# Kernel tuning notes

Measured on AMD Instinct MI355X. Metric: run time of the kernel, lower is better.

Reference implementation:

```python
import jax, jax.numpy as jnp
import numpy as np

NUM_USERS = 50000
NUM_ITEMS = 50000
LATENT_DIM = 64
NUM_INTERACTIONS = 1600000
N_LAYERS = 4  # 4 ODE blocks, euler 1-step each == 4 LightGCN propagations


def setup_inputs() -> dict:
    key = jax.random.key(0)
    k1, k2, k3, k4, k5 = jax.random.split(key, 5)
    user_emb = 0.1 * jax.random.normal(k1, (NUM_USERS, LATENT_DIM), dtype=jnp.float32)
    item_emb = 0.1 * jax.random.normal(k2, (NUM_ITEMS, LATENT_DIM), dtype=jnp.float32)
    eu = jax.random.randint(k3, (NUM_INTERACTIONS,), 0, NUM_USERS, dtype=jnp.int32)
    ei = jax.random.randint(jax.random.fold_in(k3, 1), (NUM_INTERACTIONS,), 0, NUM_ITEMS, dtype=jnp.int32)
    edge_index = jnp.stack([eu, ei])  # [2, E] user->item interactions
    users = jax.random.randint(k4, (4096,), 0, NUM_USERS, dtype=jnp.int32)
    items = jax.random.randint(k5, (4096,), 0, NUM_ITEMS, dtype=jnp.int32)
    return {"user_emb": user_emb, "item_emb": item_emb,
            "edge_index": edge_index, "users": users, "items": items}


def _graph(edge_index):
    # Symmetric bipartite graph over n_users + n_items nodes, normalized D^-1/2 A D^-1/2.
    eu, ei = edge_index[0], edge_index[1] + NUM_USERS
    rows = jnp.concatenate([eu, ei])
    cols = jnp.concatenate([ei, eu])
    n = NUM_USERS + NUM_ITEMS
    deg = jax.ops.segment_sum(jnp.ones_like(rows, dtype=jnp.float32), rows, num_segments=n)
    dinv = jnp.where(deg > 0, jax.lax.rsqrt(jnp.maximum(deg, 1.0)), 0.0)
    w = dinv[rows] * dinv[cols]  # [2E]
    return rows, cols, w


def _propagate(x, rows, cols, w):
    # sparse matmul: out[r] += w_e * x[c]  (irregular gather + segment-sum)
    n = NUM_USERS + NUM_ITEMS
    return jax.ops.segment_sum(x[cols] * w[:, None], rows, num_segments=n)


def _computer(user_emb, item_emb, edge_index):
    rows, cols, w = _graph(edge_index)
    e0 = jnp.concatenate([user_emb, item_emb])  # [N, d]
    # fixed-time euler: block_k(x) = x + A x; residual subtraction leaves A x
    embs = [e0]
    x = e0
    for _ in range(N_LAYERS):
        x = _propagate(x, rows, cols, w)
        embs.append(x)
    light_out = jnp.mean(jnp.stack(embs, axis=1), axis=1)  # [N, d]
    return light_out[:NUM_USERS], light_out[NUM_USERS:]


def reference(user_emb, item_emb, edge_index, users, items):
    all_users, all_items = _computer(user_emb, item_emb, edge_index)
    u = all_users[users]
    i = all_items[items]
    gamma = jnp.sum(u * i, axis=1)  # [B]
    return gamma
```

## Files before the change

kernel.cpp:

```cpp
#include <hip/hip_runtime.h>

#define LAT 64
#define ELLC 64
#define RB 128
#define RBSH 7
#define MAXBUK 1024
#define RPT 8

#define SC0 64.0f
#define RSC 3.0f

typedef float f32x2 __attribute__((ext_vector_type(2)));

__global__ void __launch_bounds__(1024)
bin_k(const int* __restrict__ eu, const int* __restrict__ ei,
      int* __restrict__ gcur, unsigned int* __restrict__ bbuf,
      int2* __restrict__ ovf, int* __restrict__ ovfc,
      int E, int U, int nbuk, int cap, int ovf_cap) {
    __shared__ int lcnt[MAXBUK];
    __shared__ int lbase[MAXBUK];
    for (int i = threadIdx.x; i < nbuk; i += blockDim.x) lcnt[i] = 0;
    __syncthreads();
    int tid = blockIdx.x * blockDim.x + threadIdx.x;
    int stride = gridDim.x * blockDim.x;
    int ru[RPT], rc[RPT];
    int ne = 0;
#pragma unroll
    for (int k = 0; k < RPT; ++k) {
        int d = tid + k * stride;
        if (d < E) {
            int u = eu[d], c = ei[d] + U;
            ru[k] = u; rc[k] = c; ne = k + 1;
            atomicAdd(&lcnt[u >> RBSH], 1);
            atomicAdd(&lcnt[c >> RBSH], 1);
        }
    }
    __syncthreads();
    for (int b = threadIdx.x; b < nbuk; b += blockDim.x)
        lbase[b] = atomicAdd(&gcur[b], lcnt[b]);
    __syncthreads();
#pragma unroll
    for (int k = 0; k < RPT; ++k) {
        if (k < ne) {
            int u = ru[k], c = rc[k];
            int b = u >> RBSH;
            int pos = atomicAdd(&lbase[b], 1);
            if (pos < cap)
                bbuf[(size_t)b * cap + pos] = ((unsigned)(u & (RB - 1)) << 17) | (unsigned)c;
            else { int o = atomicAdd(ovfc, 1); if (o < ovf_cap) ovf[o] = make_int2(u, c); }
            b = c >> RBSH;
            pos = atomicAdd(&lbase[b], 1);
            if (pos < cap)
                bbuf[(size_t)b * cap + pos] = ((unsigned)(c & (RB - 1)) << 17) | (unsigned)u;
            else { int o = atomicAdd(ovfc, 1); if (o < ovf_cap) ovf[o] = make_int2(c, u); }
        }
    }
}

__global__ void __launch_bounds__(1024)
build_k(const unsigned int* __restrict__ bbuf, const int* __restrict__ gcur,
        int* __restrict__ cnt, int* __restrict__ colE, float* __restrict__ dinv,
        const float* __restrict__ ue, const float* __restrict__ ie,
        unsigned char* __restrict__ y0,
        int2* __restrict__ rovf, int* __restrict__ rovfc,
        int N, int U, int cap, int rovf_cap) {
    __shared__ int lcnt[RB];
    __shared__ float ldv[RB];
    __shared__ int ell[RB * ELLC];
    int b = blockIdx.x;
    for (int i = threadIdx.x; i < RB; i += blockDim.x) lcnt[i] = 0;
    for (int i = threadIdx.x; i < RB * ELLC; i += blockDim.x) ell[i] = 0;
    __syncthreads();
    int nb = min(gcur[b], cap);
    const unsigned int* src = bbuf + (size_t)b * cap;
    for (int e = threadIdx.x; e < nb; e += blockDim.x) {
        unsigned w = src[e];
        int r7 = (int)(w >> 17);
        int c = (int)(w & 0x1FFFF);
        int pos = atomicAdd(&lcnt[r7], 1);
        if (pos < ELLC) ell[(r7 << 6) + pos] = c;
        else {
            int o = atomicAdd(rovfc, 1);
            if (o < rovf_cap) rovf[o] = make_int2((b << RBSH) + r7, c);
        }
    }
    __syncthreads();
    for (int i = threadIdx.x; i < RB; i += blockDim.x) {
        int r = (b << RBSH) + i;
        if (r < N) {
            int d = lcnt[i];
            cnt[r] = d;
            float dv = (d > 0) ? rsqrtf((float)d) : 0.0f;
            dinv[r] = dv;
            ldv[i] = dv;
        }
    }
    __syncthreads();
    int r0 = b << RBSH;
    int rows = min(RB, N - r0);
    for (int w = threadIdx.x; w < rows * 16; w += blockDim.x) {
        int i = w >> 4, j = w & 15;
        int r = r0 + i;
        const float* s = (r < U) ? (ue + (size_t)r * LAT) : (ie + (size_t)(r - U) * LAT);
        float4 f = ((const float4*)s)[j];
        float sc = SC0 * ldv[i];
        int p = __builtin_amdgcn_cvt_pk_fp8_f32(sc * f.x, sc * f.y, 0, false);
        p = __builtin_amdgcn_cvt_pk_fp8_f32(sc * f.z, sc * f.w, p, true);
        ((unsigned*)y0)[(size_t)r * 16 + j] = (unsigned)p;
    }
    uint4* dst = (uint4*)(colE + (size_t)r0 * ELLC);
    const uint4* lsrc = (const uint4*)ell;
    for (int w = threadIdx.x; w < rows * 16; w += blockDim.x)
        dst[w] = lsrc[w];
}

__global__ void __launch_bounds__(1024)
fix_k(const int2* __restrict__ ovf, const int* __restrict__ ovfc,
      int* __restrict__ cnt, int* __restrict__ colE, float* __restrict__ dinv,
      const float* __restrict__ ue, const float* __restrict__ ie,
      unsigned char* __restrict__ y0,
      int2* __restrict__ rovf, int* __restrict__ rovfc,
      int ovf_cap, int rovf_cap, int U) {
    int n = min(*ovfc, ovf_cap);
    for (int i = threadIdx.x; i < n; i += blockDim.x) {
        int r = ovf[i].x, c = ovf[i].y;
        int pos = atomicAdd(&cnt[r], 1);
        if (pos < ELLC) colE[(size_t)r * ELLC + pos] = c;
        else { int o = atomicAdd(rovfc, 1); if (o < rovf_cap) rovf[o] = make_int2(r, c); }
    }
    __syncthreads();
    for (int i = threadIdx.x; i < n; i += blockDim.x) {
        int r = ovf[i].x;
        int d = cnt[r];
        dinv[r] = (d > 0) ? rsqrtf((float)d) : 0.0f;
    }
    __syncthreads();
    for (int w = threadIdx.x; w < n * 16; w += blockDim.x) {
        int o = w >> 4, j = w & 15;
        int r = ovf[o].x;
        const float* s = (r < U) ? (ue + (size_t)r * LAT) : (ie + (size_t)(r - U) * LAT);
        float4 f = ((const float4*)s)[j];
        float sc = SC0 * dinv[r];
        int p = __builtin_amdgcn_cvt_pk_fp8_f32(sc * f.x, sc * f.y, 0, false);
        p = __builtin_amdgcn_cvt_pk_fp8_f32(sc * f.z, sc * f.w, p, true);
        ((unsigned*)y0)[(size_t)r * 16 + j] = (unsigned)p;
    }
}

__device__ __forceinline__ void acc_word(unsigned w, f32x2* a) {
    a[0] += __builtin_amdgcn_cvt_pk_f32_fp8((int)w, false);
    a[1] += __builtin_amdgcn_cvt_pk_f32_fp8((int)w, true);
}

__global__ void __launch_bounds__(256, 8)
prop_h_k(const int* __restrict__ cnt, const int* __restrict__ colE,
         const float* __restrict__ dinv, const unsigned char* __restrict__ yin,
         unsigned char* __restrict__ yout,
         const int* __restrict__ users, const int* __restrict__ items,
         float* __restrict__ qacc,
         const float* __restrict__ ue, const float* __restrict__ ie,
         const int2* __restrict__ rovf, const int* __restrict__ rovfc,
         int rovf_cap, int B, int U, int first, int N, float inv_sin) {
    int wave = blockIdx.x * (blockDim.x >> 6) + (threadIdx.x >> 6);
    int lane = threadIdx.x & 63;
    int NW = (N + 3) >> 2;
    if (wave >= NW) {
        int qw = wave - NW;
        if (qw >= 2 * B) return;
        int node = (qw < B) ? users[qw] : (items[qw - B] + U);
        if (first) {
            float v = (node < U) ? ue[(size_t)node * LAT + lane]
                                 : ie[(size_t)(node - U) * LAT + lane];
            qacc[qw * LAT + lane] = v;
        } else {
            float di = dinv[node];
            unsigned bb = yin[(size_t)node * LAT + lane];
            f32x2 yv = __builtin_amdgcn_cvt_pk_f32_fp8((int)bb, false);
            qacc[qw * LAT + lane] += (di > 0.0f) ? yv[0] * inv_sin / di : 0.0f;
        }
        return;
    }
    int grp  = lane >> 4;
    int gbase = lane & 48;
    int q  = (lane >> 2) & 3;
    int s4 = lane & 3;
    int node = (wave << 2) + grp;
    int nadr = min(node, N - 1);
    int len = (node < N) ? min(cnt[nadr], ELLC) : 0;
    const int* cp = colE + (size_t)nadr * ELLC;
    int wmax = len;
    wmax = max(wmax, __shfl_xor(wmax, 16));
    wmax = max(wmax, __shfl_xor(wmax, 32));
    wmax = __builtin_amdgcn_readfirstlane(wmax);
    int gl = lane & 15;
    int ca0 = cp[gl];
    int ca1 = (wmax > 16) ? cp[16 + gl] : 0;
    int ca2 = (wmax > 32) ? cp[32 + gl] : 0;
    int ca3 = (wmax > 48) ? cp[48 + gl] : 0;
    const uint4* y16 = (const uint4*)yin;

    f32x2 acc[8];
#pragma unroll
    for (int j = 0; j < 8; ++j) acc[j] = (f32x2)(0.f);

#pragma unroll
    for (int c = 0; c < 4; ++c) {
        int cac = (c == 0) ? ca0 : (c == 1) ? ca1 : (c == 2) ? ca2 : ca3;
#pragma unroll
        for (int si = 0; si < 4; ++si) {
            int s = (c << 2) + si;
            if ((s << 2) < wmax) {
                int col = __shfl(cac, gbase + (si << 2) + q);
                if ((s << 2) + q < len) {
                    uint4 v = y16[(size_t)col * 4 + s4];
                    acc_word(v.x, acc + 0); acc_word(v.y, acc + 2);
                    acc_word(v.z, acc + 4); acc_word(v.w, acc + 6);
                }
            }
        }
    }
    int novf = min(*rovfc, rovf_cap);
    for (int o = 0; o < novf; ++o) {
        int2 eo = rovf[o];
        if (eo.x == node && q == 0) {
            uint4 vv = y16[(size_t)eo.y * 4 + s4];
            acc_word(vv.x, acc + 0); acc_word(vv.y, acc + 2);
            acc_word(vv.z, acc + 4); acc_word(vv.w, acc + 6);
        }
    }
    {
        bool hi = (lane & 4) != 0;
        f32x2 s[4], k[4];
#pragma unroll
        for (int i = 0; i < 4; ++i) { k[i] = hi ? acc[4 + i] : acc[i]; s[i] = hi ? acc[i] : acc[4 + i]; }
#pragma unroll
        for (int i = 0; i < 4; ++i) {
            f32x2 t;
            t.x = __shfl_xor(s[i].x, 4);
            t.y = __shfl_xor(s[i].y, 4);
            acc[i] = k[i] + t;
        }
    }
    {
        bool hi = (lane & 8) != 0;
        f32x2 s[2], k[2];
#pragma unroll
        for (int i = 0; i < 2; ++i) { k[i] = hi ? acc[2 + i] : acc[i]; s[i] = hi ? acc[i] : acc[2 + i]; }
#pragma unroll
        for (int i = 0; i < 2; ++i) {
            f32x2 t;
            t.x = __shfl_xor(s[i].x, 8);
            t.y = __shfl_xor(s[i].y, 8);
            acc[i] = k[i] + t;
        }
    }
    float dv = dinv[nadr];
    float f = dv * dv * RSC;
    int pk = __builtin_amdgcn_cvt_pk_fp8_f32(f * acc[0].x, f * acc[0].y, 0, false);
    pk = __builtin_amdgcn_cvt_pk_fp8_f32(f * acc[1].x, f * acc[1].y, pk, true);
    if (node < N) {
        int b2 = (lane >> 2) & 1, b3 = (lane >> 3) & 1;
        ((unsigned*)yout)[(size_t)node * 16 + (s4 << 2) + (b2 << 1) + b3] = (unsigned)pk;
    }
}

__global__ void final_k(const float* __restrict__ qacc, const unsigned char* __restrict__ y4,
                        const float* __restrict__ dinv,
                        const int* __restrict__ users, const int* __restrict__ items,
                        float* __restrict__ out, int B, int U, float inv_s4) {
    int wave = blockIdx.x * (blockDim.x >> 6) + (threadIdx.x >> 6);
    int lane = threadIdx.x & 63;
    if (wave >= B) return;
    int un = users[wave];
    int in = items[wave] + U;
    float du = dinv[un], di = dinv[in];
    unsigned bu = y4[(size_t)un * LAT + lane];
    unsigned bi = y4[(size_t)in * LAT + lane];
    f32x2 xuv = __builtin_amdgcn_cvt_pk_f32_fp8((int)bu, false);
    f32x2 xiv = __builtin_amdgcn_cvt_pk_f32_fp8((int)bi, false);
    float au = qacc[wave * LAT + lane]       + ((du > 0.f) ? xuv[0] * inv_s4 / du : 0.f);
    float ai = qacc[(wave + B) * LAT + lane] + ((di > 0.f) ? xiv[0] * inv_s4 / di : 0.f);
    float p = au * ai;
#pragma unroll
    for (int off = 32; off > 0; off >>= 1) p += __shfl_down(p, off);
    if (lane == 0) out[wave] = p * (1.0f / 25.0f);
}

extern "C" void kernel_launch(void* const* d_in, const int* in_sizes, int n_in,
                              void* d_out, int out_size, void* d_ws, size_t ws_size,
                              hipStream_t stream) {
    const float* ue = (const float*)d_in[0];
    const float* ie = (const float*)d_in[1];
    const int* edge = (const int*)d_in[2];
    const int* users = (const int*)d_in[3];
    const int* items = (const int*)d_in[4];

    const int U = in_sizes[0] / LAT;
    const int I = in_sizes[1] / LAT;
    const int N = U + I;
    const int E = in_sizes[2] / 2;
    const int B = in_sizes[3];
    const int* eu = edge;
    const int* ei = edge + E;

    const int nbuk = (N + RB - 1) / RB;
    const int cap = ((2 * E / nbuk) * 5 / 4 + 255) & ~255;

    char* ws = (char*)d_ws;
    size_t off = 0;
    auto alloc = [&](size_t bytes) -> void* {
        void* p = ws + off;
        off += (bytes + 255) & ~(size_t)255;
        return p;
    };
    int*           cnt  = (int*)alloc((size_t)4 * N);
    float*         dinv = (float*)alloc((size_t)4 * N);
    int*           colE = (int*)alloc((size_t)4 * N * ELLC);
    unsigned char* yA   = (unsigned char*)alloc((size_t)N * LAT);
    unsigned char* yB   = (unsigned char*)alloc((size_t)N * LAT);
    float*         qacc = (float*)alloc((size_t)4 * 2 * B * LAT);
    unsigned*      bbuf = (unsigned*)alloc((size_t)4 * nbuk * cap);
    size_t zoff = off;
    int*      gcur = (int*)alloc((size_t)4 * nbuk);
    int*      ovfc = (int*)alloc(256);
    size_t zbytes = off - zoff;
    size_t remain = (ws_size > off + 256) ? (ws_size - off - 256) : 0;
    int ovf_cap = (int)min((size_t)131072, remain / (2 * sizeof(int2)));
    int2* ovf  = (int2*)alloc((size_t)ovf_cap * sizeof(int2));
    int2* rovf = (int2*)alloc((size_t)ovf_cap * sizeof(int2));
    int* rovfc = ovfc + 16;

    hipError_t _e = hipMemsetAsync(gcur, 0, zbytes, stream); (void)_e;

    const int tb = 256;

    bin_k<<<256, 1024, 0, stream>>>(eu, ei, gcur, bbuf, ovf, ovfc, E, U, nbuk, cap, ovf_cap);
    build_k<<<nbuk, 1024, 0, stream>>>(bbuf, gcur, cnt, colE, dinv, ue, ie, yA,
                                       rovf, rovfc, N, U, cap, ovf_cap);
    fix_k<<<1, 1024, 0, stream>>>(ovf, ovfc, cnt, colE, dinv, ue, ie, yA,
                                  rovf, rovfc, ovf_cap, ovf_cap, U);

    const int wpb = tb / 64;
    const int NW = (N + 3) >> 2;
    int pgrid = (NW + 2 * B + wpb - 1) / wpb;

    unsigned char* yin = yA;
    unsigned char* yout = yB;
    float s_in = SC0;
    for (int layer = 0; layer < 4; ++layer) {
        prop_h_k<<<pgrid, tb, 0, stream>>>(cnt, colE, dinv, yin, yout,
                                           users, items, qacc, ue, ie, rovf, rovfc,
                                           ovf_cap, B, U, layer == 0 ? 1 : 0, N,
                                           1.0f / s_in);
        s_in *= RSC;
        unsigned char* tmp = yin; yin = yout; yout = tmp;
    }

    final_k<<<(B + wpb - 1) / wpb, tb, 0, stream>>>(qacc, yin, dinv, users, items,
                                                    (float*)d_out, B, U, 1.0f / s_in);
}
```

Baseline: 238.7 us.

## Compute final propagation layer only for queried user and item nodes

```diff
diff --git a/kernel.cpp b/kernel.cpp
--- a/kernel.cpp
+++ b/kernel.cpp
@@ -264,22 +264,116 @@
     }
 }
 
-__global__ void final_k(const float* __restrict__ qacc, const unsigned char* __restrict__ y4,
-                        const float* __restrict__ dinv,
-                        const int* __restrict__ users, const int* __restrict__ items,
-                        float* __restrict__ out, int B, int U, float inv_s4) {
+__global__ void __launch_bounds__(256, 8)
+last_k(const int* __restrict__ cnt, const int* __restrict__ colE,
+       const float* __restrict__ dinv, const unsigned char* __restrict__ y3,
+       const int* __restrict__ users, const int* __restrict__ items,
+       float* __restrict__ qacc,
+       const int2* __restrict__ rovf, const int* __restrict__ rovfc,
+       int rovf_cap, int B, int U, int N, float inv_s3) {
+    int wave = blockIdx.x * (blockDim.x >> 6) + (threadIdx.x >> 6);
+    int lane = threadIdx.x & 63;
+    int grp  = lane >> 4;
+    int gbase = lane & 48;
+    int q  = (lane >> 2) & 3;
+    int s4 = lane & 3;
+    int e = (wave << 2) + grp;
+    int ecl = min(e, 2 * B - 1);
+    int node = (ecl < B) ? users[ecl] : (items[ecl - B] + U);
+    bool valid = (e < 2 * B);
+    int len = valid ? min(cnt[node], ELLC) : 0;
+    const int* cp = colE + (size_t)node * ELLC;
+    int wmax = len;
+    wmax = max(wmax, __shfl_xor(wmax, 16));
+    wmax = max(wmax, __shfl_xor(wmax, 32));
+    wmax = __builtin_amdgcn_readfirstlane(wmax);
+    int gl = lane & 15;
+    int ca0 = cp[gl];
+    int ca1 = (wmax > 16) ? cp[16 + gl] : 0;
+    int ca2 = (wmax > 32) ? cp[32 + gl] : 0;
+    int ca3 = (wmax > 48) ? cp[48 + gl] : 0;
+    const uint4* y16 = (const uint4*)y3;
+
+    f32x2 acc[8];
+#pragma unroll
+    for (int j = 0; j < 8; ++j) acc[j] = (f32x2)(0.f);
+
+#pragma unroll
+    for (int c = 0; c < 4; ++c) {
+        int cac = (c == 0) ? ca0 : (c == 1) ? ca1 : (c == 2) ? ca2 : ca3;
+#pragma unroll
+        for (int si = 0; si < 4; ++si) {
+            int s = (c << 2) + si;
+            if ((s << 2) < wmax) {
+                int col = __shfl(cac, gbase + (si << 2) + q);
+                if ((s << 2) + q < len) {
+                    uint4 v = y16[(size_t)col * 4 + s4];
+                    acc_word(v.x, acc + 0); acc_word(v.y, acc + 2);
+                    acc_word(v.z, acc + 4); acc_word(v.w, acc + 6);
+                }
+            }
+        }
+    }
+    int novf = min(*rovfc, rovf_cap);
+    for (int o = 0; o < novf; ++o) {
+        int2 eo = rovf[o];
+        if (valid && eo.x == node && q == 0) {
+            uint4 vv = y16[(size_t)eo.y * 4 + s4];
+            acc_word(vv.x, acc + 0); acc_word(vv.y, acc + 2);
+            acc_word(vv.z, acc + 4); acc_word(vv.w, acc + 6);
+        }
+    }
+    {
+        bool hi = (lane & 4) != 0;
+        f32x2 s[4], k[4];
+#pragma unroll
+        for (int i = 0; i < 4; ++i) { k[i] = hi ? acc[4 + i] : acc[i]; s[i] = hi ? acc[i] : acc[4 + i]; }
+#pragma unroll
+        for (int i = 0; i < 4; ++i) {
+            f32x2 t;
+            t.x = __shfl_xor(s[i].x, 4);
+            t.y = __shfl_xor(s[i].y, 4);
+            acc[i] = k[i] + t;
+        }
+    }
+    {
+        bool hi = (lane & 8) != 0;
+        f32x2 s[2], k[2];
+#pragma unroll
+        for (int i = 0; i < 2; ++i) { k[i] = hi ? acc[2 + i] : acc[i]; s[i] = hi ? acc[i] : acc[2 + i]; }
+#pragma unroll
+        for (int i = 0; i < 2; ++i) {
+            f32x2 t;
+            t.x = __shfl_xor(s[i].x, 8);
+            t.y = __shfl_xor(s[i].y, 8);
+            acc[i] = k[i] + t;
+        }
+    }
+    int b2 = (lane >> 2) & 1, b3 = (lane >> 3) & 1;
+    int widx = (s4 << 2) + (b2 << 1) + b3;
+    float dv = dinv[node];
+    float x4s = dv * inv_s3;
+    float r3 = (dv > 0.f) ? inv_s3 / dv : 0.f;
+    unsigned w3 = ((const unsigned*)y3)[(size_t)node * 16 + widx];
+    f32x2 lo3 = __builtin_amdgcn_cvt_pk_f32_fp8((int)w3, false);
+    f32x2 hi3 = __builtin_amdgcn_cvt_pk_f32_fp8((int)w3, true);
+    if (valid) {
+        float4* qp = (float4*)(qacc + (size_t)e * LAT + (widx << 2));
+        float4 old = *qp;
+        old.x += x4s * acc[0].x + r3 * lo3[0];
+        old.y += x4s * acc[0].y + r3 * lo3[1];
+        old.z += x4s * acc[1].x + r3 * hi3[0];
+        old.w += x4s * acc[1].y + r3 * hi3[1];
+        *qp = old;
+    }
+}
+
+__global__ void dot_k(const float* __restrict__ qacc, float* __restrict__ out, int B) {
     int wave = blockIdx.x * (blockDim.x >> 6) + (threadIdx.x >> 6);
     int lane = threadIdx.x & 63;
     if (wave >= B) return;
-    int un = users[wave];
-    int in = items[wave] + U;
-    float du = dinv[un], di = dinv[in];
-    unsigned bu = y4[(size_t)un * LAT + lane];
-    unsigned bi = y4[(size_t)in * LAT + lane];
-    f32x2 xuv = __builtin_amdgcn_cvt_pk_f32_fp8((int)bu, false);
-    f32x2 xiv = __builtin_amdgcn_cvt_pk_f32_fp8((int)bi, false);
-    float au = qacc[wave * LAT + lane]       + ((du > 0.f) ? xuv[0] * inv_s4 / du : 0.f);
-    float ai = qacc[(wave + B) * LAT + lane] + ((di > 0.f) ? xiv[0] * inv_s4 / di : 0.f);
+    float au = qacc[(size_t)wave * LAT + lane];
+    float ai = qacc[(size_t)(wave + B) * LAT + lane];
     float p = au * ai;
 #pragma unroll
     for (int off = 32; off > 0; off >>= 1) p += __shfl_down(p, off);
@@ -347,7 +441,7 @@
     unsigned char* yin = yA;
     unsigned char* yout = yB;
     float s_in = SC0;
-    for (int layer = 0; layer < 4; ++layer) {
+    for (int layer = 0; layer < 3; ++layer) {
         prop_h_k<<<pgrid, tb, 0, stream>>>(cnt, colE, dinv, yin, yout,
                                            users, items, qacc, ue, ie, rovf, rovfc,
                                            ovf_cap, B, U, layer == 0 ? 1 : 0, N,
@@ -356,6 +450,11 @@
         unsigned char* tmp = yin; yin = yout; yout = tmp;
     }
 
-    final_k<<<(B + wpb - 1) / wpb, tb, 0, stream>>>(qacc, yin, dinv, users, items,
-                                                    (float*)d_out, B, U, 1.0f / s_in);
-}
+    int lwaves = (2 * B + 3) >> 2;
+    last_k<<<(lwaves + wpb - 1) / wpb, tb, 0, stream>>>(cnt, colE, dinv, yin,
+                                                        users, items, qacc,
+                                                        rovf, rovfc, ovf_cap,
+                                                        B, U, N, 1.0f / s_in);
+
+    dot_k<<<(B + wpb - 1) / wpb, tb, 0, stream>>>(qacc, (float*)d_out, B);
+}
```

Result: faster. 218.3 us (median of 2 runs) (-8.5%).
